# Kernel optimization log

Hardware: AMD Instinct MI355X
Metric: run time of the kernel (lower is better)

Reference implementation:

```python
import jax, jax.numpy as jnp
import numpy as np

N = 50000
E = 800000
IN_DIM = 256
OUT_DIM = 128
HEADS = 4
D_K = OUT_DIM // HEADS  # 32
BETA = 1.0  # beta_init, requires_grad=False (constant)
NEG_SLOPE = 0.2
EPS = 1e-12


def setup_inputs() -> dict:
    key = jax.random.key(0)
    k = jax.random.split(key, 8)
    H = jax.random.normal(k[0], (N, IN_DIM), dtype=jnp.float32)
    edge_index = jax.random.randint(k[1], (2, E), 0, N, dtype=jnp.int64)
    sim1_edge = jax.random.normal(k[2], (E,), dtype=jnp.float32)
    # Parameters (torch nn.Linear stores weight as (out, in); y = x @ W.T)
    W = jax.random.normal(k[3], (HEADS * D_K, IN_DIM), dtype=jnp.float32) * (1.0 / np.sqrt(IN_DIM))
    a_src = jax.random.normal(k[4], (HEADS, D_K), dtype=jnp.float32)
    a_dst = jax.random.normal(k[5], (HEADS, D_K), dtype=jnp.float32)
    msg_lin_w = jax.random.normal(k[6], (D_K, D_K), dtype=jnp.float32) * (1.0 / np.sqrt(D_K))
    return {"H": H, "edge_index": edge_index, "sim1_edge": sim1_edge,
            "W": W, "a_src": a_src, "a_dst": a_dst, "msg_lin_w": msg_lin_w}


def reference(H, edge_index, sim1_edge, W, a_src, a_dst, msg_lin_w):
    n = H.shape[0]
    H_proj = (H @ W.T).reshape(n, HEADS, D_K)           # [N, h, d_k]
    src, dst = edge_index[0], edge_index[1]
    h_src = H_proj[src]                                  # [E, h, d_k]
    h_dst = H_proj[dst]                                  # [E, h, d_k]
    # per-edge attention logits (struct + semantic)
    e = (jnp.einsum('ehd,hd->eh', h_src, a_src)
         + jnp.einsum('ehd,hd->eh', h_dst, a_dst)
         + BETA * sim1_edge[:, None])                    # [E, h]
    e = jnp.where(e >= 0, e, NEG_SLOPE * e)              # LeakyReLU(0.2)
    # global (per-head) max for stabilization, matching original e.max(dim=0)
    e = e - jnp.max(e, axis=0, keepdims=True)
    exp_e = jnp.exp(e)                                   # [E, h]
    denom = jax.ops.segment_sum(exp_e, dst, num_segments=n)  # [N, h]
    alpha = exp_e / (denom[dst] + EPS)                   # [E, h]  (dropout p=0 -> identity)
    m = alpha[:, :, None] * h_src                        # [E, h, d_k]
    out = jax.ops.segment_sum(m, dst, num_segments=n)    # [N, h, d_k]
    out_h = out.reshape(n, HEADS * D_K)                  # concat=True
    msg_base = jnp.einsum('ehd,od->eho', h_src, msg_lin_w).mean(axis=1)  # [E, d_k]
    alpha_mean = alpha.mean(axis=1)                      # [E]
    return out_h, alpha_mean, msg_base
```

## Files before the change

kernel.cpp:

```cpp
#include <hip/hip_runtime.h>
#include <hip/hip_bf16.h>
#include <hip/hip_fp16.h>
#include <float.h>

#define HEADS 4
#define DK 32

static constexpr float kBeta = 1.0f;
static constexpr float kNeg  = 0.2f;
static constexpr float kEps  = 1e-12f;

typedef __bf16 bf16x8 __attribute__((ext_vector_type(8)));
typedef float  f32x4  __attribute__((ext_vector_type(4)));

__device__ __forceinline__ float bf2f(unsigned short v) {
  return __uint_as_float((unsigned)v << 16);
}
__device__ __forceinline__ unsigned short f2bf(float f) {
  unsigned u = __float_as_uint(f);
  unsigned r = u + 0x7FFFu + ((u >> 16) & 1u);
  return (unsigned short)(r >> 16);
}
__device__ __forceinline__ unsigned fkey(float x) {
  unsigned u = __float_as_uint(x);
  return (u & 0x80000000u) ? ~u : (u | 0x80000000u);
}
__device__ __forceinline__ float funkey(unsigned k) {
  unsigned u = (k & 0x80000000u) ? (k & 0x7fffffffu) : ~k;
  return __uint_as_float(u);
}
__device__ __forceinline__ bf16x8 as8(uint4 v) {
  union { uint4 u; bf16x8 b; } x; x.u = v; return x.b;
}

__global__ __launch_bounds__(256) void k_detect(const int* __restrict__ ei32,
                                                const unsigned* __restrict__ Hw,
                                                int* __restrict__ eflag,
                                                int* __restrict__ dflag,
                                                int E, int nw) {
  int i = blockIdx.x * 256 + threadIdx.x;
  if (i < 4096 && 2 * i + 1 < 2 * E && ei32[2 * i + 1] != 0) atomicOr(eflag, 1);
  if (i < nw && ((Hw[i] >> 7) & 0xFFu) == 0xFFu) atomicOr(dflag, 1);
}

__global__ __launch_bounds__(256) void k_cvt(const int* __restrict__ ei32,
                                             const int* __restrict__ eflag,
                                             int* __restrict__ src_i,
                                             int* __restrict__ dst_i,
                                             int* __restrict__ deg, int E) {
  int i = blockIdx.x * 256 + threadIdx.x;
  if (i >= E) return;
  int s, d;
  if (*eflag) { s = ei32[i];     d = ei32[E + i]; }
  else        { s = ei32[2 * i]; d = ei32[2 * E + 2 * i]; }
  src_i[i] = s;
  dst_i[i] = d;
  atomicAdd(deg + d, 1);
}

__global__ __launch_bounds__(256) void k_wparams(const void* __restrict__ in,
                                                 unsigned short* __restrict__ Bhi,
                                                 unsigned short* __restrict__ Blo,
                                                 const void* __restrict__ a_src,
                                                 const void* __restrict__ a_dst,
                                                 const void* __restrict__ msg_w,
                                                 float* __restrict__ af,
                                                 float* __restrict__ msgwf,
                                                 const int* __restrict__ dflag) {
  const int dt = *dflag;
  if (blockIdx.x < 128) {
    int i = blockIdx.x * 256 + threadIdx.x;
    int r = i >> 8, c = i & 255;
    float v = dt ? ((const float*)in)[i] : bf2f(((const unsigned short*)in)[i]);
    unsigned short hb = f2bf(v);
    unsigned short lb = f2bf(v - bf2f(hb));
    int kt = c >> 5, ct = r >> 4;
    int lane = (((c >> 3) & 3) << 4) | (r & 15);
    int idx = ((kt * 8 + ct) * 64 + lane) * 8 + (c & 7);
    Bhi[idx] = hb;
    Blo[idx] = lb;
  } else {
    int i = (blockIdx.x - 128) * 256 + threadIdx.x;
    if (i < 128) {
      af[i] = dt ? ((const float*)a_src)[i] : bf2f(((const unsigned short*)a_src)[i]);
    } else if (i < 256) {
      int j = i - 128;
      af[i] = dt ? ((const float*)a_dst)[j] : bf2f(((const unsigned short*)a_dst)[j]);
    } else if (i < 1280) {
      int j = i - 256;
      msgwf[j] = dt ? ((const float*)msg_w)[j] : bf2f(((const unsigned short*)msg_w)[j]);
    }
  }
}

__global__ __launch_bounds__(256) void k_scan1(const int* __restrict__ deg,
                                               int* __restrict__ bsum, int N) {
  const int t = threadIdx.x;
  int i = blockIdx.x * 256 + t;
  int v = (i < N) ? deg[i] : 0;
#pragma unroll
  for (int off = 32; off; off >>= 1) v += __shfl_xor(v, off);
  __shared__ int red[4];
  if ((t & 63) == 0) red[t >> 6] = v;
  __syncthreads();
  if (t == 0) bsum[blockIdx.x] = red[0] + red[1] + red[2] + red[3];
}
__global__ __launch_bounds__(1024) void k_scan2(int* __restrict__ bsum, int nb) {
  __shared__ int part[1024];
  const int t = threadIdx.x;
  part[t] = (t < nb) ? bsum[t] : 0;
  __syncthreads();
  int own = part[t];
  for (int off = 1; off < 1024; off <<= 1) {
    int v = (t >= off) ? part[t - off] : 0;
    __syncthreads();
    part[t] += v;
    __syncthreads();
  }
  if (t < nb) bsum[t] = part[t] - own;
}
__global__ __launch_bounds__(256) void k_scan3(const int* __restrict__ deg,
                                               const int* __restrict__ bsum,
                                               int* __restrict__ row_ptr,
                                               int* __restrict__ cursor, int N) {
  __shared__ int part[256];
  const int t = threadIdx.x;
  int i = blockIdx.x * 256 + t;
  int v = (i < N) ? deg[i] : 0;
  part[t] = v;
  __syncthreads();
  for (int off = 1; off < 256; off <<= 1) {
    int x = (t >= off) ? part[t - off] : 0;
    __syncthreads();
    part[t] += x;
    __syncthreads();
  }
  int excl = part[t] - v + bsum[blockIdx.x];
  if (i < N) {
    row_ptr[i] = excl;
    cursor[i]  = excl;
    if (i == N - 1) row_ptr[N] = excl + v;
  }
}

__global__ __launch_bounds__(256) void k_proj(const void* __restrict__ Hraw,
                                              const unsigned short* __restrict__ Bhi,
                                              const unsigned short* __restrict__ Blo,
                                              const int* __restrict__ dflag,
                                              const float* __restrict__ af,
                                              const float* __restrict__ msgwf,
                                              float* __restrict__ s_src,
                                              float* __restrict__ s_dst,
                                              __half* __restrict__ msgb,
                                              __half* __restrict__ Hb, int N) {
  __shared__ uint4 ldsA[2048];
  __shared__ uint4 ldsB[2048];
  float* ldsF = (float*)ldsA;
  const int t = threadIdx.x;
  const int nb = blockIdx.x * 64;
  const int dt = *dflag;
  const int l = t & 63;
  const int wv = t >> 6;
  const int wrow = wv * 16;
  const int c16 = l & 15;
  const int g4 = l >> 4;

  f32x4 acc[8];
#pragma unroll
  for (int ct = 0; ct < 8; ++ct) acc[ct] = (f32x4){0.f, 0.f, 0.f, 0.f};
  const uint4* __restrict__ Bh4 = (const uint4*)Bhi;
  const uint4* __restrict__ Bl4 = (const uint4*)Blo;

  if (!dt) {
    const uint4* __restrict__ H8 = (const uint4*)Hraw;
#pragma unroll
    for (int it = 0; it < 8; ++it) {
      int c = it * 256 + t;
      int row = c >> 5, k8 = c & 31;
      int gr = nb + row;
      uint4 v = make_uint4(0u, 0u, 0u, 0u);
      if (gr < N) v = H8[(size_t)gr * 32 + k8];
      ldsA[(k8 * 64 + row) ^ (k8 & 7)] = v;
    }
#pragma unroll
    for (int it = 0; it < 8; ++it) ldsB[it * 256 + t] = Bh4[it * 256 + t];
    __syncthreads();
#pragma unroll
    for (int kt = 0; kt < 4; ++kt) {
      int k8 = kt * 4 + g4;
      int slot = (k8 * 64 + wrow + c16) ^ (k8 & 7);
      bf16x8 ah = as8(ldsA[slot]);
#pragma unroll
      for (int ct = 0; ct < 8; ++ct) {
        bf16x8 bh = as8(ldsB[(kt * 8 + ct) * 64 + l]);
        acc[ct] = __builtin_amdgcn_mfma_f32_16x16x32_bf16(ah, bh, acc[ct], 0, 0, 0);
      }
    }
    __syncthreads();
#pragma unroll
    for (int it = 0; it < 8; ++it) ldsB[it * 256 + t] = Bh4[2048 + it * 256 + t];
    __syncthreads();
#pragma unroll
    for (int kt = 4; kt < 8; ++kt) {
      int k8 = kt * 4 + g4;
      int slot = (k8 * 64 + wrow + c16) ^ (k8 & 7);
      bf16x8 ah = as8(ldsA[slot]);
#pragma unroll
      for (int ct = 0; ct < 8; ++ct) {
        bf16x8 bh = as8(ldsB[((kt - 4) * 8 + ct) * 64 + l]);
        acc[ct] = __builtin_amdgcn_mfma_f32_16x16x32_bf16(ah, bh, acc[ct], 0, 0, 0);
      }
    }
  } else {
    const float4* __restrict__ H4 = (const float4*)Hraw;
#pragma unroll
    for (int it = 0; it < 8; ++it) {
      int c = it * 256 + t;
      int row = c >> 5, k8 = c & 31;
      int gr = nb + row;
      float4 v0 = make_float4(0.f, 0.f, 0.f, 0.f), v1 = v0;
      if (gr < N) {
        v0 = H4[(size_t)gr * 64 + k8 * 2];
        v1 = H4[(size_t)gr * 64 + k8 * 2 + 1];
      }
      float f[8] = {v0.x, v0.y, v0.z, v0.w, v1.x, v1.y, v1.z, v1.w};
      unsigned hi[8];
#pragma unroll
      for (int j = 0; j < 8; ++j) hi[j] = f2bf(f[j]);
      ldsA[(k8 * 64 + row) ^ (k8 & 7)] =
          make_uint4(hi[0] | (hi[1] << 16), hi[2] | (hi[3] << 16),
                     hi[4] | (hi[5] << 16), hi[6] | (hi[7] << 16));
    }
    __syncthreads();
#pragma unroll 2
    for (int kt = 0; kt < 8; ++kt) {
      int k8 = kt * 4 + g4;
      int slot = (k8 * 64 + wrow + c16) ^ (k8 & 7);
      bf16x8 ah = as8(ldsA[slot]);
#pragma unroll
      for (int ct = 0; ct < 8; ++ct) {
        bf16x8 bh = as8(Bh4[(kt * 8 + ct) * 64 + l]);
        acc[ct] = __builtin_amdgcn_mfma_f32_16x16x32_bf16(ah, bh, acc[ct], 0, 0, 0);
        bf16x8 bl = as8(Bl4[(kt * 8 + ct) * 64 + l]);
        acc[ct] = __builtin_amdgcn_mfma_f32_16x16x32_bf16(ah, bl, acc[ct], 0, 0, 0);
      }
    }
    __syncthreads();
#pragma unroll
    for (int it = 0; it < 8; ++it) {
      int c = it * 256 + t;
      int row = c >> 5, k8 = c & 31;
      int gr = nb + row;
      float4 v0 = make_float4(0.f, 0.f, 0.f, 0.f), v1 = v0;
      if (gr < N) {
        v0 = H4[(size_t)gr * 64 + k8 * 2];
        v1 = H4[(size_t)gr * 64 + k8 * 2 + 1];
      }
      float f[8] = {v0.x, v0.y, v0.z, v0.w, v1.x, v1.y, v1.z, v1.w};
      unsigned lo[8];
#pragma unroll
      for (int j = 0; j < 8; ++j) lo[j] = f2bf(f[j] - bf2f(f2bf(f[j])));
      ldsA[(k8 * 64 + row) ^ (k8 & 7)] =
          make_uint4(lo[0] | (lo[1] << 16), lo[2] | (lo[3] << 16),
                     lo[4] | (lo[5] << 16), lo[6] | (lo[7] << 16));
    }
    __syncthreads();
#pragma unroll 2
    for (int kt = 0; kt < 8; ++kt) {
      int k8 = kt * 4 + g4;
      int slot = (k8 * 64 + wrow + c16) ^ (k8 & 7);
      bf16x8 al = as8(ldsA[slot]);
#pragma unroll
      for (int ct = 0; ct < 8; ++ct) {
        bf16x8 bh = as8(Bh4[(kt * 8 + ct) * 64 + l]);
        acc[ct] = __builtin_amdgcn_mfma_f32_16x16x32_bf16(al, bh, acc[ct], 0, 0, 0);
      }
    }
  }
  __syncthreads();

#pragma unroll
  for (int i = 0; i < 4; ++i) {
    int idx = t * 4 + i;
    ldsF[(idx >> 5) * 33 + (idx & 31)] = msgwf[idx];
  }
  float* hbuf = ldsF + 1056 + wv * 528;
#pragma unroll
  for (int r = 0; r < 4; ++r) {
    float h0 = 0.25f * (acc[0][r] + acc[2][r] + acc[4][r] + acc[6][r]);
    float h1 = 0.25f * (acc[1][r] + acc[3][r] + acc[5][r] + acc[7][r]);
    hbuf[(g4 * 4 + r) * 33 + c16]      = h0;
    hbuf[(g4 * 4 + r) * 33 + 16 + c16] = h1;
  }
  __syncthreads();

  float afp[8], afq[8];
#pragma unroll
  for (int ct = 0; ct < 8; ++ct) {
    afp[ct] = af[ct * 16 + c16];
    afq[ct] = af[128 + ct * 16 + c16];
  }
  float pv0[4], pv1[4], pv2[4], pv3[4], qv0[4], qv1[4], qv2[4], qv3[4];
#pragma unroll
  for (int r = 0; r < 4; ++r) {
    pv0[r] = acc[0][r] * afp[0] + acc[1][r] * afp[1];
    pv1[r] = acc[2][r] * afp[2] + acc[3][r] * afp[3];
    pv2[r] = acc[4][r] * afp[4] + acc[5][r] * afp[5];
    pv3[r] = acc[6][r] * afp[6] + acc[7][r] * afp[7];
    qv0[r] = acc[0][r] * afq[0] + acc[1][r] * afq[1];
    qv1[r] = acc[2][r] * afq[2] + acc[3][r] * afq[3];
    qv2[r] = acc[4][r] * afq[4] + acc[5][r] * afq[5];
    qv3[r] = acc[6][r] * afq[6] + acc[7][r] * afq[7];
  }
#pragma unroll
  for (int off = 1; off <= 8; off <<= 1) {
#pragma unroll
    for (int r = 0; r < 4; ++r) {
      pv0[r] += __shfl_xor(pv0[r], off);
      pv1[r] += __shfl_xor(pv1[r], off);
      pv2[r] += __shfl_xor(pv2[r], off);
      pv3[r] += __shfl_xor(pv3[r], off);
      qv0[r] += __shfl_xor(qv0[r], off);
      qv1[r] += __shfl_xor(qv1[r], off);
      qv2[r] += __shfl_xor(qv2[r], off);
      qv3[r] += __shfl_xor(qv3[r], off);
    }
  }
#pragma unroll
  for (int r = 0; r < 4; ++r) {
    int n = nb + wrow + g4 * 4 + r;
    if (n < N) {
      if (c16 < 4) {
        float v = (c16 == 0) ? pv0[r] : (c16 == 1) ? pv1[r]
                 : (c16 == 2) ? pv2[r] : pv3[r];
        s_src[(size_t)n * 4 + c16] = v;
      } else if (c16 < 8) {
        int hh = c16 - 4;
        float v = (hh == 0) ? qv0[r] : (hh == 1) ? qv1[r]
                 : (hh == 2) ? qv2[r] : qv3[r];
        s_dst[(size_t)n * 4 + hh] = v;
      }
    }
  }
#pragma unroll
  for (int ct = 0; ct < 8; ++ct) {
#pragma unroll
    for (int r = 0; r < 4; ++r) {
      int n = nb + wrow + g4 * 4 + r;
      if (n < N) Hb[(size_t)n * 128 + ct * 16 + c16] = __float2half(acc[ct][r]);
    }
  }
  {
    const int j = l & 31;
    const int r0 = (l >> 5) * 8;
    float res[8] = {0.f, 0.f, 0.f, 0.f, 0.f, 0.f, 0.f, 0.f};
#pragma unroll 4
    for (int d = 0; d < 32; ++d) {
      float mw = ldsF[j * 33 + d];
#pragma unroll
      for (int i = 0; i < 8; ++i) res[i] += hbuf[(r0 + i) * 33 + d] * mw;
    }
#pragma unroll
    for (int i = 0; i < 8; ++i) {
      int n = nb + wrow + r0 + i;
      if (n < N) msgb[(size_t)n * 32 + j] = __float2half(res[i]);
    }
  }
}

__global__ __launch_bounds__(256) void k_fillog(const int* __restrict__ src,
                                                const int* __restrict__ dstv,
                                                const void* __restrict__ sim1,
                                                const int* __restrict__ dflag,
                                                const float* __restrict__ s_src,
                                                const float* __restrict__ s_dst,
                                                int* __restrict__ cursor,
                                                int2* __restrict__ pack,
                                                unsigned* __restrict__ gmax, int E) {
  const int e = blockIdx.x * 256 + threadIdx.x;
  float m0 = -FLT_MAX, m1 = -FLT_MAX, m2 = -FLT_MAX, m3 = -FLT_MAX;
  if (e < E) {
    int s = src[e], d = dstv[e];
    float sv = (*dflag) ? ((const float*)sim1)[e] : bf2f(((const unsigned short*)sim1)[e]);
    int pos = atomicAdd(cursor + d, 1);
    pack[pos] = make_int2(s, __float_as_int(sv));
    float4 ss = *(const float4*)(s_src + (size_t)s * 4);
    float4 sd = *(const float4*)(s_dst + (size_t)d * 4);
    float b = kBeta * sv;
    float e0 = ss.x + sd.x + b; e0 = (e0 >= 0.f) ? e0 : kNeg * e0;
    float e1 = ss.y + sd.y + b; e1 = (e1 >= 0.f) ? e1 : kNeg * e1;
    float e2 = ss.z + sd.z + b; e2 = (e2 >= 0.f) ? e2 : kNeg * e2;
    float e3 = ss.w + sd.w + b; e3 = (e3 >= 0.f) ? e3 : kNeg * e3;
    m0 = e0; m1 = e1; m2 = e2; m3 = e3;
  }
#pragma unroll
  for (int off = 32; off; off >>= 1) {
    m0 = fmaxf(m0, __shfl_xor(m0, off));
    m1 = fmaxf(m1, __shfl_xor(m1, off));
    m2 = fmaxf(m2, __shfl_xor(m2, off));
    m3 = fmaxf(m3, __shfl_xor(m3, off));
  }
  __shared__ float red[4][4];
  if ((threadIdx.x & 63) == 0) {
    int w = threadIdx.x >> 6;
    red[w][0] = m0; red[w][1] = m1; red[w][2] = m2; red[w][3] = m3;
  }
  __syncthreads();
  if (threadIdx.x < 4) {
    int h = threadIdx.x;
    float mm = fmaxf(fmaxf(red[0][h], red[1][h]), fmaxf(red[2][h], red[3][h]));
    atomicMax(gmax + h, fkey(mm));
  }
}

__global__ __launch_bounds__(256) void k_out(const int* __restrict__ row_ptr,
                                             const int2* __restrict__ pack,
                                             const float* __restrict__ s_src,
                                             const float* __restrict__ s_dst,
                                             const unsigned* __restrict__ gmax,
                                             const unsigned* __restrict__ Hb_u,
                                             const int* __restrict__ dflag,
                                             float* __restrict__ denom,
                                             void* __restrict__ d_out, int N) {
  const int n = (int)((blockIdx.x * 256 + threadIdx.x) >> 6);
  const int l = threadIdx.x & 63;
  if (n >= N) return;
  const int beg = row_ptr[n];
  const int deg = row_ptr[n + 1] - beg;
  const int dt = *dflag;
  const float m0 = funkey(gmax[0]), m1 = funkey(gmax[1]);
  const float m2 = funkey(gmax[2]), m3 = funkey(gmax[3]);
  const float4 sd = *(const float4*)(s_dst + (size_t)n * 4);
  float accx = 0.f, accy = 0.f;
  float4 dn = make_float4(0.f, 0.f, 0.f, 0.f);
  int s = 0;
  float4 ev = make_float4(0.f, 0.f, 0.f, 0.f);
  const bool small = (deg <= 64);
  if (small) {
    if (l < deg) {
      int2 p = pack[beg + l];
      s = p.x;
      float sv = __int_as_float(p.y);
      float4 ss = *(const float4*)(s_src + (size_t)s * 4);
      float e0 = ss.x + sd.x + sv; e0 = (e0 >= 0.f) ? e0 : kNeg * e0;
      float e1 = ss.y + sd.y + sv; e1 = (e1 >= 0.f) ? e1 : kNeg * e1;
      float e2 = ss.z + sd.z + sv; e2 = (e2 >= 0.f) ? e2 : kNeg * e2;
      float e3 = ss.w + sd.w + sv; e3 = (e3 >= 0.f) ? e3 : kNeg * e3;
      ev = make_float4(expf(e0 - m0), expf(e1 - m1), expf(e2 - m2), expf(e3 - m3));
      dn = ev;
    }
  } else {
    for (int base = 0; base < deg; base += 64) {
      if (base + l < deg) {
        int2 p = pack[beg + base + l];
        float sv = __int_as_float(p.y);
        float4 ss = *(const float4*)(s_src + (size_t)p.x * 4);
        float e0 = ss.x + sd.x + sv; e0 = (e0 >= 0.f) ? e0 : kNeg * e0;
        float e1 = ss.y + sd.y + sv; e1 = (e1 >= 0.f) ? e1 : kNeg * e1;
        float e2 = ss.z + sd.z + sv; e2 = (e2 >= 0.f) ? e2 : kNeg * e2;
        float e3 = ss.w + sd.w + sv; e3 = (e3 >= 0.f) ? e3 : kNeg * e3;
        dn.x += expf(e0 - m0); dn.y += expf(e1 - m1);
        dn.z += expf(e2 - m2); dn.w += expf(e3 - m3);
      }
    }
  }
#pragma unroll
  for (int off = 32; off; off >>= 1) {
    dn.x += __shfl_xor(dn.x, off);
    dn.y += __shfl_xor(dn.y, off);
    dn.z += __shfl_xor(dn.z, off);
    dn.w += __shfl_xor(dn.w, off);
  }
  if (l == 0) *(float4*)(denom + (size_t)n * 4) = make_float4(dn.x, dn.y, dn.z, dn.w);
  const float i0 = 1.f / (dn.x + kEps), i1 = 1.f / (dn.y + kEps);
  const float i2 = 1.f / (dn.z + kEps), i3 = 1.f / (dn.w + kEps);
  const float myinv = (l < 32) ? ((l < 16) ? i0 : i1) : ((l < 48) ? i2 : i3);
  if (small) {
    for (int i = 0; i < deg; ++i) {
      int si = __shfl(s, i);
      float ax = __shfl(ev.x, i), ay = __shfl(ev.y, i);
      float az = __shfl(ev.z, i), aw = __shfl(ev.w, i);
      float aa = ((l < 32) ? ((l < 16) ? ax : ay) : ((l < 48) ? az : aw)) * myinv;
      unsigned u = Hb_u[(size_t)si * 64 + l];
      float2 f = __half22float2(*(const __half2*)&u);
      accx += aa * f.x;
      accy += aa * f.y;
    }
  } else {
    for (int base = 0; base < deg; base += 64) {
      int cnt = min(64, deg - base);
      int s2 = 0;
      float4 e2v = make_float4(0.f, 0.f, 0.f, 0.f);
      if (l < cnt) {
        int2 p = pack[beg + base + l];
        s2 = p.x;
        float sv = __int_as_float(p.y);
        float4 ss = *(const float4*)(s_src + (size_t)s2 * 4);
        float e0 = ss.x + sd.x + sv; e0 = (e0 >= 0.f) ? e0 : kNeg * e0;
        float e1 = ss.y + sd.y + sv; e1 = (e1 >= 0.f) ? e1 : kNeg * e1;
        float e2 = ss.z + sd.z + sv; e2 = (e2 >= 0.f) ? e2 : kNeg * e2;
        float e3 = ss.w + sd.w + sv; e3 = (e3 >= 0.f) ? e3 : kNeg * e3;
        e2v = make_float4(expf(e0 - m0), expf(e1 - m1), expf(e2 - m2), expf(e3 - m3));
      }
      for (int i = 0; i < cnt; ++i) {
        int si = __shfl(s2, i);
        float ax = __shfl(e2v.x, i), ay = __shfl(e2v.y, i);
        float az = __shfl(e2v.z, i), aw = __shfl(e2v.w, i);
        float aa = ((l < 32) ? ((l < 16) ? ax : ay) : ((l < 48) ? az : aw)) * myinv;
        unsigned u = Hb_u[(size_t)si * 64 + l];
        float2 f = __half22float2(*(const __half2*)&u);
        accx += aa * f.x;
        accy += aa * f.y;
      }
    }
  }
  if (dt) {
    *(float2*)&((float*)d_out)[(size_t)n * 128 + 2 * l] = make_float2(accx, accy);
  } else {
    __hip_bfloat162 b = __float22bfloat162_rn(make_float2(accx, accy));
    *(__hip_bfloat162*)((__hip_bfloat16*)d_out + (size_t)n * 128 + 2 * l) = b;
  }
}

__global__ __launch_bounds__(256) void k_edge(const int* __restrict__ src,
                                              const int* __restrict__ dstv,
                                              const void* __restrict__ sim1,
                                              const int* __restrict__ dflag,
                                              const float* __restrict__ s_src,
                                              const float* __restrict__ s_dst,
                                              const float* __restrict__ denom,
                                              const unsigned* __restrict__ gmax,
                                              const __half2* __restrict__ msgb2,
                                              void* __restrict__ d_out,
                                              int N, int E) {
  long long tid = (long long)blockIdx.x * 256 + threadIdx.x;
  if (tid >= (long long)E * 16) return;
  int e = (int)(tid >> 4), jp = (int)(tid & 15);
  const int dt = *dflag;
  int s = src[e];
  __half2 hv = msgb2[(size_t)s * 16 + jp];
  float2 f = __half22float2(hv);
  const size_t alpha_off = (size_t)N * 128;
  const size_t msg_off = alpha_off + (size_t)E;
  if (dt) {
    *(float2*)&((float*)d_out)[msg_off + (size_t)e * 32 + 2 * jp] = f;
  } else {
    __hip_bfloat162 b = __float22bfloat162_rn(f);
    *(__hip_bfloat162*)((__hip_bfloat16*)d_out + msg_off + (size_t)e * 32 + 2 * jp) = b;
  }
  if (jp == 0) {
    int d = dstv[e];
    float sv = dt ? ((const float*)sim1)[e] : bf2f(((const unsigned short*)sim1)[e]);
    float4 ss = *(const float4*)(s_src + (size_t)s * 4);
    float4 sd = *(const float4*)(s_dst + (size_t)d * 4);
    float4 dn = *(const float4*)(denom + (size_t)d * 4);
    float m0 = funkey(gmax[0]), m1 = funkey(gmax[1]);
    float m2 = funkey(gmax[2]), m3 = funkey(gmax[3]);
    float b = kBeta * sv;
    float e0 = ss.x + sd.x + b; e0 = (e0 >= 0.f) ? e0 : kNeg * e0;
    float e1 = ss.y + sd.y + b; e1 = (e1 >= 0.f) ? e1 : kNeg * e1;
    float e2 = ss.z + sd.z + b; e2 = (e2 >= 0.f) ? e2 : kNeg * e2;
    float e3 = ss.w + sd.w + b; e3 = (e3 >= 0.f) ? e3 : kNeg * e3;
    float am = 0.25f * (expf(e0 - m0) / (dn.x + kEps) + expf(e1 - m1) / (dn.y + kEps) +
                        expf(e2 - m2) / (dn.z + kEps) + expf(e3 - m3) / (dn.w + kEps));
    if (dt) ((float*)d_out)[alpha_off + e] = am;
    else    ((__hip_bfloat16*)d_out)[alpha_off + e] = __float2bfloat16(am);
  }
}

extern "C" void kernel_launch(void* const* d_in, const int* in_sizes, int n_in,
                              void* d_out, int out_size, void* d_ws, size_t ws_size,
                              hipStream_t stream) {
  const void* H     = d_in[0];
  const int*  ei    = (const int*)d_in[1];
  const void* sim1  = d_in[2];
  const void* W     = d_in[3];
  const void* a_src = d_in[4];
  const void* a_dst = d_in[5];
  const void* msg_w = d_in[6];
  const int N = in_sizes[0] / 256;
  const int E = in_sizes[2];
  const int NB = (N + 255) / 256;

  char* base     = (char*)d_ws;
  float* s_src   = (float*)base;  base += (size_t)N * 4 * 4;
  float* s_dst   = (float*)base;  base += (size_t)N * 4 * 4;
  __half* msgb   = (__half*)base; base += (size_t)N * DK * 2;
  __half* Hb     = (__half*)base; base += (size_t)N * 128 * 2;
  float* denom   = (float*)base;  base += (size_t)N * 4 * 4;
  unsigned short* Bhi = (unsigned short*)base; base += 32768 * 2;
  unsigned short* Blo = (unsigned short*)base; base += 32768 * 2;
  int* deg       = (int*)base;    base += (size_t)N * 4;
  unsigned* gmax = (unsigned*)base; base += 4 * 4;
  int* eflag     = (int*)base;    base += 4;
  int* dflag     = (int*)base;    base += 4;
  int* row_ptr   = (int*)base;    base += (size_t)(N + 2) * 4;
  int* cursor    = (int*)base;    base += (size_t)N * 4;
  int* bsum      = (int*)base;    base += 1024 * 4;
  int2* pack     = (int2*)base;   base += (size_t)E * 8;
  int* src_i     = (int*)base;    base += (size_t)E * 4;
  int* dst_i     = (int*)base;    base += (size_t)E * 4;
  float* af      = (float*)base;  base += 256 * 4;
  float* msgwf   = (float*)base;  base += 1024 * 4;

  hipMemsetAsync(deg, 0, (size_t)(N + 6) * sizeof(int), stream);

  k_detect<<<512, 256, 0, stream>>>(ei, (const unsigned*)H, eflag, dflag, E, 131072);
  k_cvt<<<(E + 255) / 256, 256, 0, stream>>>(ei, eflag, src_i, dst_i, deg, E);
  k_wparams<<<133, 256, 0, stream>>>(W, Bhi, Blo, a_src, a_dst, msg_w, af, msgwf, dflag);
  k_proj<<<(N + 63) / 64, 256, 0, stream>>>(H, Bhi, Blo, dflag, af, msgwf,
                                            s_src, s_dst, msgb, Hb, N);
  k_scan1<<<NB, 256, 0, stream>>>(deg, bsum, N);
  k_scan2<<<1, 1024, 0, stream>>>(bsum, NB);
  k_scan3<<<NB, 256, 0, stream>>>(deg, bsum, row_ptr, cursor, N);
  k_fillog<<<(E + 255) / 256, 256, 0, stream>>>(src_i, dst_i, sim1, dflag, s_src, s_dst,
                                                cursor, pack, gmax, E);
  k_out<<<(int)(((size_t)N * 64 + 255) / 256), 256, 0, stream>>>(
      row_ptr, pack, s_src, s_dst, gmax, (const unsigned*)Hb, dflag, denom, d_out, N);
  k_edge<<<(int)(((long long)E * 16 + 255) / 256), 256, 0, stream>>>(
      src_i, dst_i, sim1, dflag, s_src, s_dst, denom, gmax, (const __half2*)msgb,
      d_out, N, E);
}
```

Measured before the change: 469.6 us.

## Split msg_base projection into separate kernel and shrink k_proj LDS footprint

Moves the per-node msg_lin projection out of k_proj into a new k_msgb kernel, which reads the fp16 Hb output and uses wave shuffles. The B-operand LDS buffer is halved and loaded in four stages instead of two. The aim is to cut k_proj's LDS use and epilogue work so more blocks fit per CU. The cost is an extra launch and an extra read of Hb. msg_base is now computed from fp16-rounded projections rather than fp32 accumulators, which slightly changes precision.

New measurement: 492.4 us. 1.05x slower.

```diff
diff --git a/kernel.cpp b/kernel.cpp
--- a/kernel.cpp
+++ b/kernel.cpp
@@ -148,20 +148,16 @@
                                               const unsigned short* __restrict__ Blo,
                                               const int* __restrict__ dflag,
                                               const float* __restrict__ af,
-                                              const float* __restrict__ msgwf,
                                               float* __restrict__ s_src,
                                               float* __restrict__ s_dst,
-                                              __half* __restrict__ msgb,
                                               __half* __restrict__ Hb, int N) {
   __shared__ uint4 ldsA[2048];
-  __shared__ uint4 ldsB[2048];
-  float* ldsF = (float*)ldsA;
+  __shared__ uint4 ldsB[1024];
   const int t = threadIdx.x;
   const int nb = blockIdx.x * 64;
   const int dt = *dflag;
   const int l = t & 63;
-  const int wv = t >> 6;
-  const int wrow = wv * 16;
+  const int wrow = (t >> 6) * 16;
   const int c16 = l & 15;
   const int g4 = l >> 4;
 
@@ -183,32 +179,22 @@
       ldsA[(k8 * 64 + row) ^ (k8 & 7)] = v;
     }
 #pragma unroll
-    for (int it = 0; it < 8; ++it) ldsB[it * 256 + t] = Bh4[it * 256 + t];
-    __syncthreads();
-#pragma unroll
-    for (int kt = 0; kt < 4; ++kt) {
-      int k8 = kt * 4 + g4;
-      int slot = (k8 * 64 + wrow + c16) ^ (k8 & 7);
-      bf16x8 ah = as8(ldsA[slot]);
-#pragma unroll
-      for (int ct = 0; ct < 8; ++ct) {
-        bf16x8 bh = as8(ldsB[(kt * 8 + ct) * 64 + l]);
-        acc[ct] = __builtin_amdgcn_mfma_f32_16x16x32_bf16(ah, bh, acc[ct], 0, 0, 0);
-      }
-    }
-    __syncthreads();
-#pragma unroll
-    for (int it = 0; it < 8; ++it) ldsB[it * 256 + t] = Bh4[2048 + it * 256 + t];
-    __syncthreads();
-#pragma unroll
-    for (int kt = 4; kt < 8; ++kt) {
-      int k8 = kt * 4 + g4;
-      int slot = (k8 * 64 + wrow + c16) ^ (k8 & 7);
-      bf16x8 ah = as8(ldsA[slot]);
-#pragma unroll
-      for (int ct = 0; ct < 8; ++ct) {
-        bf16x8 bh = as8(ldsB[((kt - 4) * 8 + ct) * 64 + l]);
-        acc[ct] = __builtin_amdgcn_mfma_f32_16x16x32_bf16(ah, bh, acc[ct], 0, 0, 0);
+    for (int p = 0; p < 4; ++p) {
+      if (p) __syncthreads();
+#pragma unroll
+      for (int it = 0; it < 4; ++it) ldsB[it * 256 + t] = Bh4[p * 1024 + it * 256 + t];
+      __syncthreads();
+#pragma unroll
+      for (int kk = 0; kk < 2; ++kk) {
+        int kt = p * 2 + kk;
+        int k8 = kt * 4 + g4;
+        int slot = (k8 * 64 + wrow + c16) ^ (k8 & 7);
+        bf16x8 ah = as8(ldsA[slot]);
+#pragma unroll
+        for (int ct = 0; ct < 8; ++ct) {
+          bf16x8 bh = as8(ldsB[(kk * 8 + ct) * 64 + l]);
+          acc[ct] = __builtin_amdgcn_mfma_f32_16x16x32_bf16(ah, bh, acc[ct], 0, 0, 0);
+        }
       }
     }
   } else {
@@ -277,22 +263,6 @@
       }
     }
   }
-  __syncthreads();
-
-#pragma unroll
-  for (int i = 0; i < 4; ++i) {
-    int idx = t * 4 + i;
-    ldsF[(idx >> 5) * 33 + (idx & 31)] = msgwf[idx];
-  }
-  float* hbuf = ldsF + 1056 + wv * 528;
-#pragma unroll
-  for (int r = 0; r < 4; ++r) {
-    float h0 = 0.25f * (acc[0][r] + acc[2][r] + acc[4][r] + acc[6][r]);
-    float h1 = 0.25f * (acc[1][r] + acc[3][r] + acc[5][r] + acc[7][r]);
-    hbuf[(g4 * 4 + r) * 33 + c16]      = h0;
-    hbuf[(g4 * 4 + r) * 33 + 16 + c16] = h1;
-  }
-  __syncthreads();
 
   float afp[8], afq[8];
 #pragma unroll
@@ -350,21 +320,24 @@
       if (n < N) Hb[(size_t)n * 128 + ct * 16 + c16] = __float2half(acc[ct][r]);
     }
   }
-  {
-    const int j = l & 31;
-    const int r0 = (l >> 5) * 8;
-    float res[8] = {0.f, 0.f, 0.f, 0.f, 0.f, 0.f, 0.f, 0.f};
-#pragma unroll 4
-    for (int d = 0; d < 32; ++d) {
-      float mw = ldsF[j * 33 + d];
-#pragma unroll
-      for (int i = 0; i < 8; ++i) res[i] += hbuf[(r0 + i) * 33 + d] * mw;
-    }
-#pragma unroll
-    for (int i = 0; i < 8; ++i) {
-      int n = nb + wrow + r0 + i;
-      if (n < N) msgb[(size_t)n * 32 + j] = __float2half(res[i]);
-    }
+}
+
+__global__ __launch_bounds__(256) void k_msgb(const __half* __restrict__ Hb,
+                                              const float* __restrict__ msgwf,
+                                              __half* __restrict__ msgb, int N) {
+  const int l = threadIdx.x & 63;
+  const int wb = threadIdx.x >> 6;
+  const int n = (blockIdx.x << 2) + wb;
+  if (n >= N) return;
+  float h0 = __half2float(Hb[(size_t)n * 128 + l]);
+  float h1 = __half2float(Hb[(size_t)n * 128 + 64 + l]);
+  float t4 = h0 + __shfl_xor(h0, 32) + h1 + __shfl_xor(h1, 32);
+  float hbar = 0.25f * t4;
+  if (l < DK) {
+    float acc = 0.f;
+#pragma unroll
+    for (int d = 0; d < DK; ++d) acc += __shfl(hbar, d) * msgwf[l * DK + d];
+    msgb[(size_t)n * DK + l] = __float2half(acc);
   }
 }
 
@@ -608,8 +581,9 @@
   k_detect<<<512, 256, 0, stream>>>(ei, (const unsigned*)H, eflag, dflag, E, 131072);
   k_cvt<<<(E + 255) / 256, 256, 0, stream>>>(ei, eflag, src_i, dst_i, deg, E);
   k_wparams<<<133, 256, 0, stream>>>(W, Bhi, Blo, a_src, a_dst, msg_w, af, msgwf, dflag);
-  k_proj<<<(N + 63) / 64, 256, 0, stream>>>(H, Bhi, Blo, dflag, af, msgwf,
-                                            s_src, s_dst, msgb, Hb, N);
+  k_proj<<<(N + 63) / 64, 256, 0, stream>>>(H, Bhi, Blo, dflag, af,
+                                            s_src, s_dst, Hb, N);
+  k_msgb<<<(N + 3) / 4, 256, 0, stream>>>(Hb, msgwf, msgb, N);
   k_scan1<<<NB, 256, 0, stream>>>(deg, bsum, N);
   k_scan2<<<1, 1024, 0, stream>>>(bsum, NB);
   k_scan3<<<NB, 256, 0, stream>>>(deg, bsum, row_ptr, cursor, N);
```
